# Kernel tuning notes

Hardware: AMD Instinct MI355X
Metric: run time of the kernel (lower is better)

The kernel has to match this reference:

```python
import jax, jax.numpy as jnp
import numpy as np

N_NODES = 10000
N_EDGES = 640000
IN_FEATS = 256
H_FEATS = 128
NUM_CLASSES = 64


def _kaiming(key, shape):
    fan_in = shape[1]
    std = np.sqrt(2.0 / fan_in)
    return jax.random.normal(key, shape, dtype=jnp.float32) * std


def setup_inputs() -> dict:
    key = jax.random.key(0)
    ks = jax.random.split(key, 10)
    x = jax.random.normal(ks[0], (N_NODES, IN_FEATS), dtype=jnp.float32)
    edge_index = jax.random.randint(ks[1], (2, N_EDGES), 0, N_NODES, dtype=jnp.int64)
    return {
        "x": x,
        "edge_index": edge_index,
        "W_lin": _kaiming(ks[2], (H_FEATS, IN_FEATS)),
        "b_lin": jnp.zeros((H_FEATS,), jnp.float32),
        "Wl1": _kaiming(ks[3], (H_FEATS, H_FEATS)),
        "bl1": jnp.zeros((H_FEATS,), jnp.float32),
        "Wr1": _kaiming(ks[4], (H_FEATS, H_FEATS)),
        "Wl2": _kaiming(ks[5], (H_FEATS, H_FEATS)),
        "bl2": jnp.zeros((H_FEATS,), jnp.float32),
        "Wr2": _kaiming(ks[6], (H_FEATS, H_FEATS)),
        "W_cls": _kaiming(ks[7], (NUM_CLASSES, H_FEATS)),
    }


def _sage_conv(x, src, dst, Wl, bl, Wr, n_nodes):
    # PyG SAGEConv (mean aggr): out = lin_l(mean_{j->i} x_j) + lin_r(x_i)
    msg = x[src]                                    # [E, H] gather
    agg = jax.ops.segment_sum(msg, dst, num_segments=n_nodes)  # [N, H]
    deg = jax.ops.segment_sum(jnp.ones((src.shape[0],), x.dtype), dst,
                              num_segments=n_nodes)            # [N]
    mean = agg / jnp.maximum(deg, 1.0)[:, None]
    return mean @ Wl.T + bl + x @ Wr.T


def reference(x, edge_index, W_lin, b_lin, Wl1, bl1, Wr1, Wl2, bl2, Wr2, W_cls):
    src, dst = edge_index[0], edge_index[1]
    n = x.shape[0]
    h = jax.nn.relu(x @ W_lin.T + b_lin)            # input projection + relu
    h = _sage_conv(h, src, dst, Wl1, bl1, Wr1, n)   # sage1 (no relu: linear is truthy)
    h = _sage_conv(h, src, dst, Wl2, bl2, Wr2, n)   # sage2
    h = jax.nn.relu(h)
    return h @ W_cls.T                              # weight.mm(x.t()).t()
```

## Files before the change

kernel.cpp:

```cpp
#include <hip/hip_runtime.h>

#define NN 10000
#define HF 128
#define INF_ 256
#define CLS 64
#define NR 8
#define SEG 32
#define CAPT (NR * SEG)
#define NP 10240
#define RT  (NN / 16)
#define NPB 8
#define NB  (NN / NPB)
#define LDP (HF + 8)

typedef __attribute__((ext_vector_type(8))) short short8;
typedef __attribute__((ext_vector_type(4))) float f32x4;

__device__ __forceinline__ unsigned short f2bf(float f) {
    unsigned u = __builtin_bit_cast(unsigned, f);
    u = (u + 0x7fffu + ((u >> 16) & 1u)) >> 16;
    return (unsigned short)u;
}
__device__ __forceinline__ float bfbits2f(unsigned u) {
    u <<= 16;
    return __builtin_bit_cast(float, u);
}


template <int K, int NC>
__device__ __forceinline__
void mfma_rows16(int row0, int col0,
                 const unsigned short* __restrict__ A, int lda,
                 const unsigned short* __restrict__ W, f32x4* acc) {
    int lane = threadIdx.x & 63;
    int m = lane & 15, quad = lane >> 4;
    const unsigned short* arow = A + (size_t)(row0 + m) * lda + quad * 8;
    const short8* bp[NC];
#pragma unroll
    for (int c = 0; c < NC; ++c)
        bp[c] = (const short8*)(W + (size_t)(col0 + c * 16 + m) * K + quad * 8);
#pragma unroll
    for (int k0 = 0; k0 < K; k0 += 32) {
        short8 a = *(const short8*)(arow + k0);
#pragma unroll
        for (int c = 0; c < NC; ++c)
            acc[c] = __builtin_amdgcn_mfma_f32_16x16x32_bf16(a, bp[c][k0 >> 3], acc[c], 0, 0, 0);
    }
}

__device__ __forceinline__ short8 pack8(float4 a, float4 b) {
    short8 r;
    r[0] = (short)f2bf(a.x); r[1] = (short)f2bf(a.y);
    r[2] = (short)f2bf(a.z); r[3] = (short)f2bf(a.w);
    r[4] = (short)f2bf(b.x); r[5] = (short)f2bf(b.y);
    r[6] = (short)f2bf(b.z); r[7] = (short)f2bf(b.w);
    return r;
}

__device__ __forceinline__
void gemm1_wave(int row_tile, int col0, const float* __restrict__ x,
                const float* __restrict__ Wlin, const float* __restrict__ blin,
                unsigned short* __restrict__ h0) {
    int lane = threadIdx.x & 63;
    int m = lane & 15, quad = lane >> 4;
    const float* ar = x    + (size_t)(row_tile * 16 + m) * INF_ + quad * 8;
    const float* w0 = Wlin + (size_t)(col0 +  0 + m) * INF_ + quad * 8;
    const float* w1 = Wlin + (size_t)(col0 + 16 + m) * INF_ + quad * 8;
    const float* w2 = Wlin + (size_t)(col0 + 32 + m) * INF_ + quad * 8;
    const float* w3 = Wlin + (size_t)(col0 + 48 + m) * INF_ + quad * 8;
    f32x4 acc[4] = {};
#pragma unroll
    for (int k0 = 0; k0 < INF_; k0 += 32) {
        short8 a  = pack8(*(const float4*)(ar + k0), *(const float4*)(ar + k0 + 4));
        short8 b0 = pack8(*(const float4*)(w0 + k0), *(const float4*)(w0 + k0 + 4));
        short8 b1 = pack8(*(const float4*)(w1 + k0), *(const float4*)(w1 + k0 + 4));
        short8 b2 = pack8(*(const float4*)(w2 + k0), *(const float4*)(w2 + k0 + 4));
        short8 b3 = pack8(*(const float4*)(w3 + k0), *(const float4*)(w3 + k0 + 4));
        acc[0] = __builtin_amdgcn_mfma_f32_16x16x32_bf16(a, b0, acc[0], 0, 0, 0);
        acc[1] = __builtin_amdgcn_mfma_f32_16x16x32_bf16(a, b1, acc[1], 0, 0, 0);
        acc[2] = __builtin_amdgcn_mfma_f32_16x16x32_bf16(a, b2, acc[2], 0, 0, 0);
        acc[3] = __builtin_amdgcn_mfma_f32_16x16x32_bf16(a, b3, acc[3], 0, 0, 0);
    }
#pragma unroll
    for (int c = 0; c < 4; ++c) {
        int colg = col0 + c * 16 + m;
        float bv = blin[colg];
#pragma unroll
        for (int r = 0; r < 4; ++r) {
            int rowg = row_tile * 16 + quad * 4 + r;
            h0[(size_t)rowg * HF + colg] = f2bf(fmaxf(acc[c][r] + bv, 0.f));
        }
    }
}

#define GB 313
#define FB 2500
#define CB 288

__global__ __launch_bounds__(256)
void fused_k(const float* __restrict__ x, const float* __restrict__ Wlin,
             const float* __restrict__ blin, unsigned short* __restrict__ h0,
             const int* __restrict__ src, const int* __restrict__ dst,
             int* __restrict__ cnt8, unsigned short* __restrict__ colb, int E,
             const float* __restrict__ Wl1, const float* __restrict__ Wr1,
             const float* __restrict__ Wl2, const float* __restrict__ Wr2,
             const float* __restrict__ Wcls, unsigned short* __restrict__ wb) {
    int b = blockIdx.x;
    if (b < GB) {
        int wave = threadIdx.x >> 6;
        int row_tile = b * 2 + (wave >> 1);
        if (row_tile >= RT) return;
        gemm1_wave(row_tile, (wave & 1) * 64, x, Wlin, blin, h0);
    } else if (b < GB + FB) {
        int r = b & 7;
        int i = (b - GB) * 256 + threadIdx.x;
        if (i < E) {
            int d = dst[i];
            int pos = atomicAdd(&cnt8[r * NP + d], 1);
            if (pos < SEG) colb[(size_t)d * CAPT + r * SEG + pos] = (unsigned short)src[i];
        }
    } else {
        int i = (b - GB - FB) * 256 + threadIdx.x;
        const float* s; int off;
        if      (i < 16384) { s = Wl1;  off = 0; }
        else if (i < 32768) { s = Wr1;  off = 16384; }
        else if (i < 49152) { s = Wl2;  off = 32768; }
        else if (i < 65536) { s = Wr2;  off = 49152; }
        else if (i < 73728) { s = Wcls; off = 65536; }
        else return;
        wb[i] = f2bf(s[i - off]);
    }
}

__device__ __forceinline__
void gather_mean(const unsigned short* __restrict__ h,
                 const int* __restrict__ cnt8, int node,
                 const unsigned short* __restrict__ seg,
                 unsigned short* __restrict__ cols,
                 unsigned short* __restrict__ msrow) {
    int lane = threadIdx.x & 63;
    int q   = lane >> 4;
    int r16 = lane & 15;

    int craw0 = 0;
    if (lane < 8) craw0 = cnt8[lane * NP + node];
    int c0 = craw0 > SEG ? SEG : craw0;
    int off0 = 0, deg = 0, cdeg = 0;
#pragma unroll
    for (int i = 0; i < 8; ++i) {
        int ci = __shfl(c0, i);
        int ri = __shfl(craw0, i);
        if (lane > i) off0 += ci;
        cdeg += ci;
        deg  += ri;
    }
#pragma unroll
    for (int p = 0; p < 4; ++p) {
        int r = 2 * p + (lane >> 5);
        int j = lane & 31;
        unsigned short v = seg[r * SEG + j];
        int cr  = __shfl(c0, r);
        int orr = __shfl(off0, r);
        if (j < cr) cols[orr + j] = v;
    }

    const uint4* __restrict__ hp = (const uint4*)h;
    float a0 = 0.f, a1 = 0.f, a2 = 0.f, a3 = 0.f;
    float a4 = 0.f, a5 = 0.f, a6 = 0.f, a7 = 0.f;
#pragma unroll 4
    for (int e0 = 0; e0 < cdeg; e0 += 4) {
        int e = e0 + q;
        if (e < cdeg) {
            int s = (int)cols[e];
            uint4 v = hp[(size_t)s * 16 + r16];
            a0 += bfbits2f(v.x & 0xffffu); a1 += bfbits2f(v.x >> 16);
            a2 += bfbits2f(v.y & 0xffffu); a3 += bfbits2f(v.y >> 16);
            a4 += bfbits2f(v.z & 0xffffu); a5 += bfbits2f(v.z >> 16);
            a6 += bfbits2f(v.w & 0xffffu); a7 += bfbits2f(v.w >> 16);
        }
    }
    a0 += __shfl_xor(a0, 16); a0 += __shfl_xor(a0, 32);
    a1 += __shfl_xor(a1, 16); a1 += __shfl_xor(a1, 32);
    a2 += __shfl_xor(a2, 16); a2 += __shfl_xor(a2, 32);
    a3 += __shfl_xor(a3, 16); a3 += __shfl_xor(a3, 32);
    a4 += __shfl_xor(a4, 16); a4 += __shfl_xor(a4, 32);
    a5 += __shfl_xor(a5, 16); a5 += __shfl_xor(a5, 32);
    a6 += __shfl_xor(a6, 16); a6 += __shfl_xor(a6, 32);
    a7 += __shfl_xor(a7, 16); a7 += __shfl_xor(a7, 32);
    if (q == 0) {
        float inv = (deg > 0) ? 1.0f / (float)deg : 0.f;
        uint4 o;
        o.x = (unsigned)f2bf(a0 * inv) | ((unsigned)f2bf(a1 * inv) << 16);
        o.y = (unsigned)f2bf(a2 * inv) | ((unsigned)f2bf(a3 * inv) << 16);
        o.z = (unsigned)f2bf(a4 * inv) | ((unsigned)f2bf(a5 * inv) << 16);
        o.w = (unsigned)f2bf(a6 * inv) | ((unsigned)f2bf(a7 * inv) << 16);
        ((uint4*)msrow)[r16] = o;
    }
}

__global__ __launch_bounds__(512)
void aggfin1_k(const unsigned short* __restrict__ h0, const int* __restrict__ cnt8,
               const unsigned short* __restrict__ colb,
               const unsigned short* __restrict__ Wr, const unsigned short* __restrict__ Wl,
               const float* __restrict__ bias, unsigned short* __restrict__ h1) {
    __shared__ __align__(16) unsigned short ms[16][LDP];
    __shared__ __align__(16) unsigned short colsLds[NPB][CAPT];
    int wave = threadIdx.x >> 6;
    int lane = threadIdx.x & 63;
    int m = lane & 15, quad = lane >> 4;
    int row0 = blockIdx.x * NPB;
    int node = row0 + wave;
    gather_mean(h0, cnt8, node, colb + (size_t)node * CAPT,
                &colsLds[wave][0], &ms[wave][0]);

    f32x4 acc[1] = {};
    mfma_rows16<HF, 1>(row0, wave * 16, h0, HF, Wr, acc);
    __syncthreads();
    mfma_rows16<HF, 1>(0, wave * 16, &ms[0][0], LDP, Wl, acc);
    if (quad < 2) {
        int colg = wave * 16 + m;
        float bv = bias[colg];
#pragma unroll
        for (int r = 0; r < 4; ++r) {
            int rowg = row0 + quad * 4 + r;
            h1[(size_t)rowg * HF + colg] = f2bf(acc[0][r] + bv);
        }
    }
}

__global__ __launch_bounds__(512)
void aggfin2cls_k(const unsigned short* __restrict__ h1, const int* __restrict__ cnt8,
                  const unsigned short* __restrict__ colb,
                  const unsigned short* __restrict__ Wr, const unsigned short* __restrict__ Wl,
                  const float* __restrict__ bias, const unsigned short* __restrict__ Wc,
                  float* __restrict__ out) {
    __shared__ __align__(16) unsigned short ms[16][LDP];
    __shared__ __align__(16) unsigned short h2s[16][LDP];
    __shared__ __align__(16) unsigned short colsLds[NPB][CAPT];
    int wave = threadIdx.x >> 6;
    int lane = threadIdx.x & 63;
    int m = lane & 15, quad = lane >> 4;
    int row0 = blockIdx.x * NPB;
    int node = row0 + wave;
    gather_mean(h1, cnt8, node, colb + (size_t)node * CAPT,
                &colsLds[wave][0], &ms[wave][0]);

    f32x4 acc[1] = {};
    mfma_rows16<HF, 1>(row0, wave * 16, h1, HF, Wr, acc);
    __syncthreads();
    mfma_rows16<HF, 1>(0, wave * 16, &ms[0][0], LDP, Wl, acc);
    {
        int colg = wave * 16 + m;
        float bv = bias[colg];
#pragma unroll
        for (int r = 0; r < 4; ++r) {
            h2s[quad * 4 + r][colg] = f2bf(fmaxf(acc[0][r] + bv, 0.f));
        }
    }
    __syncthreads();
    if (wave < 4) {
        f32x4 cacc[1] = {};
        mfma_rows16<HF, 1>(0, wave * 16, &h2s[0][0], LDP, Wc, cacc);
        if (quad < 2) {
            int colg = wave * 16 + m;
#pragma unroll
            for (int r = 0; r < 4; ++r) {
                int rowg = row0 + quad * 4 + r;
                out[(size_t)rowg * CLS + colg] = cacc[0][r];
            }
        }
    }
}


extern "C" void kernel_launch(void* const* d_in, const int* in_sizes, int n_in,
                              void* d_out, int out_size, void* d_ws, size_t ws_size,
                              hipStream_t stream) {
    const float* x      = (const float*)d_in[0];
    const int*   ei     = (const int*)d_in[1];
    const float* W_lin  = (const float*)d_in[2];
    const float* b_lin  = (const float*)d_in[3];
    const float* Wl1    = (const float*)d_in[4];
    const float* bl1    = (const float*)d_in[5];
    const float* Wr1    = (const float*)d_in[6];
    const float* Wl2    = (const float*)d_in[7];
    const float* bl2    = (const float*)d_in[8];
    const float* Wr2    = (const float*)d_in[9];
    const float* W_cls  = (const float*)d_in[10];
    float* out = (float*)d_out;

    const int E = in_sizes[1] / 2;
    const int* src = ei;
    const int* dst = ei + E;

    unsigned short* wb  = (unsigned short*)d_ws;
    unsigned short* wbl1 = wb;
    unsigned short* wbr1 = wb + 16384;
    unsigned short* wbl2 = wb + 32768;
    unsigned short* wbr2 = wb + 49152;
    unsigned short* wbc  = wb + 65536;
    unsigned short* h0  = wb + 73728;
    unsigned short* h1  = h0 + (size_t)(NN + 16) * HF;
    int* cnt8 = (int*)(h1 + (size_t)(NN + 16) * HF);
    unsigned short* colb = (unsigned short*)(cnt8 + NR * NP);

    hipMemsetAsync(cnt8, 0, NR * NP * sizeof(int), stream);

    fused_k<<<GB + FB + CB, 256, 0, stream>>>(
        x, W_lin, b_lin, h0, src, dst, cnt8, colb, E,
        Wl1, Wr1, Wl2, Wr2, W_cls, wb);

    aggfin1_k<<<NB, 512, 0, stream>>>(h0, cnt8, colb, wbr1, wbl1, bl1, h1);

    aggfin2cls_k<<<NB, 512, 0, stream>>>(h1, cnt8, colb, wbr2, wbl2, bl2, wbc, out);
}
```

Baseline: 176.3 us.

## Process 16 nodes per block with two interleaved gathers per wave

Each 512-thread block now handles 16 nodes instead of 8, with each wave gathering and averaging neighbor features for two nodes in an interleaved loop. The 16-row MFMA tiles are now fully used instead of half-wasted, and the block count is halved. The interleaving puts more independent loads in flight per wave, at the cost of more registers and load imbalance between the paired nodes. The h0/h1 padding was removed because 10000 divides evenly by 16.

```diff
diff --git a/kernel.cpp b/kernel.cpp
--- a/kernel.cpp
+++ b/kernel.cpp
@@ -9,8 +9,6 @@
 #define CAPT (NR * SEG)
 #define NP 10240
 #define RT  (NN / 16)
-#define NPB 8
-#define NB  (NN / NPB)
 #define LDP (HF + 8)
 
 typedef __attribute__((ext_vector_type(8))) short short8;
@@ -29,12 +27,12 @@
 
 template <int K, int NC>
 __device__ __forceinline__
-void mfma_rows16(int row0, int col0,
-                 const unsigned short* __restrict__ A, int lda,
-                 const unsigned short* __restrict__ W, f32x4* acc) {
+void mfma_cols(int row_tile, int col0,
+               const unsigned short* __restrict__ A, int lda,
+               const unsigned short* __restrict__ W, f32x4* acc) {
     int lane = threadIdx.x & 63;
     int m = lane & 15, quad = lane >> 4;
-    const unsigned short* arow = A + (size_t)(row0 + m) * lda + quad * 8;
+    const unsigned short* arow = A + (size_t)(row_tile * 16 + m) * lda + quad * 8;
     const short8* bp[NC];
 #pragma unroll
     for (int c = 0; c < NC; ++c)
@@ -133,19 +131,14 @@
 }
 
 __device__ __forceinline__
-void gather_mean(const unsigned short* __restrict__ h,
-                 const int* __restrict__ cnt8, int node,
-                 const unsigned short* __restrict__ seg,
-                 unsigned short* __restrict__ cols,
-                 unsigned short* __restrict__ msrow) {
-    int lane = threadIdx.x & 63;
-    int q   = lane >> 4;
-    int r16 = lane & 15;
-
+void compact_node(const int* __restrict__ cnt8, int node,
+                  const unsigned short* __restrict__ seg,
+                  unsigned short* __restrict__ cols, int& cdeg, int& deg) {
+    int lane = threadIdx.x & 63;
     int craw0 = 0;
     if (lane < 8) craw0 = cnt8[lane * NP + node];
     int c0 = craw0 > SEG ? SEG : craw0;
-    int off0 = 0, deg = 0, cdeg = 0;
+    int off0 = 0; cdeg = 0; deg = 0;
 #pragma unroll
     for (int i = 0; i < 8; ++i) {
         int ci = __shfl(c0, i);
@@ -163,20 +156,45 @@
         int orr = __shfl(off0, r);
         if (j < cr) cols[orr + j] = v;
     }
+}
+
+__device__ __forceinline__
+void gather2(const unsigned short* __restrict__ h,
+             const int* __restrict__ cnt8, int nodeA, int nodeB,
+             const unsigned short* __restrict__ colb,
+             unsigned short* __restrict__ colsA, unsigned short* __restrict__ colsB,
+             unsigned short* __restrict__ msA, unsigned short* __restrict__ msB) {
+    int lane = threadIdx.x & 63;
+    int q   = lane >> 4;
+    int r16 = lane & 15;
+    int cdA, dgA, cdB, dgB;
+    compact_node(cnt8, nodeA, colb + (size_t)nodeA * CAPT, colsA, cdA, dgA);
+    compact_node(cnt8, nodeB, colb + (size_t)nodeB * CAPT, colsB, cdB, dgB);
 
     const uint4* __restrict__ hp = (const uint4*)h;
     float a0 = 0.f, a1 = 0.f, a2 = 0.f, a3 = 0.f;
     float a4 = 0.f, a5 = 0.f, a6 = 0.f, a7 = 0.f;
+    float b0 = 0.f, b1 = 0.f, b2 = 0.f, b3 = 0.f;
+    float b4 = 0.f, b5 = 0.f, b6 = 0.f, b7 = 0.f;
+    int cdmax = cdA > cdB ? cdA : cdB;
 #pragma unroll 4
-    for (int e0 = 0; e0 < cdeg; e0 += 4) {
+    for (int e0 = 0; e0 < cdmax; e0 += 4) {
         int e = e0 + q;
-        if (e < cdeg) {
-            int s = (int)cols[e];
+        if (e < cdA) {
+            int s = (int)colsA[e];
             uint4 v = hp[(size_t)s * 16 + r16];
             a0 += bfbits2f(v.x & 0xffffu); a1 += bfbits2f(v.x >> 16);
             a2 += bfbits2f(v.y & 0xffffu); a3 += bfbits2f(v.y >> 16);
             a4 += bfbits2f(v.z & 0xffffu); a5 += bfbits2f(v.z >> 16);
             a6 += bfbits2f(v.w & 0xffffu); a7 += bfbits2f(v.w >> 16);
+        }
+        if (e < cdB) {
+            int s = (int)colsB[e];
+            uint4 v = hp[(size_t)s * 16 + r16];
+            b0 += bfbits2f(v.x & 0xffffu); b1 += bfbits2f(v.x >> 16);
+            b2 += bfbits2f(v.y & 0xffffu); b3 += bfbits2f(v.y >> 16);
+            b4 += bfbits2f(v.z & 0xffffu); b5 += bfbits2f(v.z >> 16);
+            b6 += bfbits2f(v.w & 0xffffu); b7 += bfbits2f(v.w >> 16);
         }
     }
     a0 += __shfl_xor(a0, 16); a0 += __shfl_xor(a0, 32);
@@ -187,14 +205,28 @@
     a5 += __shfl_xor(a5, 16); a5 += __shfl_xor(a5, 32);
     a6 += __shfl_xor(a6, 16); a6 += __shfl_xor(a6, 32);
     a7 += __shfl_xor(a7, 16); a7 += __shfl_xor(a7, 32);
+    b0 += __shfl_xor(b0, 16); b0 += __shfl_xor(b0, 32);
+    b1 += __shfl_xor(b1, 16); b1 += __shfl_xor(b1, 32);
+    b2 += __shfl_xor(b2, 16); b2 += __shfl_xor(b2, 32);
+    b3 += __shfl_xor(b3, 16); b3 += __shfl_xor(b3, 32);
+    b4 += __shfl_xor(b4, 16); b4 += __shfl_xor(b4, 32);
+    b5 += __shfl_xor(b5, 16); b5 += __shfl_xor(b5, 32);
+    b6 += __shfl_xor(b6, 16); b6 += __shfl_xor(b6, 32);
+    b7 += __shfl_xor(b7, 16); b7 += __shfl_xor(b7, 32);
     if (q == 0) {
-        float inv = (deg > 0) ? 1.0f / (float)deg : 0.f;
-        uint4 o;
-        o.x = (unsigned)f2bf(a0 * inv) | ((unsigned)f2bf(a1 * inv) << 16);
-        o.y = (unsigned)f2bf(a2 * inv) | ((unsigned)f2bf(a3 * inv) << 16);
-        o.z = (unsigned)f2bf(a4 * inv) | ((unsigned)f2bf(a5 * inv) << 16);
-        o.w = (unsigned)f2bf(a6 * inv) | ((unsigned)f2bf(a7 * inv) << 16);
-        ((uint4*)msrow)[r16] = o;
+        float ia = (dgA > 0) ? 1.0f / (float)dgA : 0.f;
+        float ib = (dgB > 0) ? 1.0f / (float)dgB : 0.f;
+        uint4 oa, ob;
+        oa.x = (unsigned)f2bf(a0 * ia) | ((unsigned)f2bf(a1 * ia) << 16);
+        oa.y = (unsigned)f2bf(a2 * ia) | ((unsigned)f2bf(a3 * ia) << 16);
+        oa.z = (unsigned)f2bf(a4 * ia) | ((unsigned)f2bf(a5 * ia) << 16);
+        oa.w = (unsigned)f2bf(a6 * ia) | ((unsigned)f2bf(a7 * ia) << 16);
+        ob.x = (unsigned)f2bf(b0 * ib) | ((unsigned)f2bf(b1 * ib) << 16);
+        ob.y = (unsigned)f2bf(b2 * ib) | ((unsigned)f2bf(b3 * ib) << 16);
+        ob.z = (unsigned)f2bf(b4 * ib) | ((unsigned)f2bf(b5 * ib) << 16);
+        ob.w = (unsigned)f2bf(b6 * ib) | ((unsigned)f2bf(b7 * ib) << 16);
+        ((uint4*)msA)[r16] = oa;
+        ((uint4*)msB)[r16] = ob;
     }
 }
 
@@ -204,25 +236,25 @@
                const unsigned short* __restrict__ Wr, const unsigned short* __restrict__ Wl,
                const float* __restrict__ bias, unsigned short* __restrict__ h1) {
     __shared__ __align__(16) unsigned short ms[16][LDP];
-    __shared__ __align__(16) unsigned short colsLds[NPB][CAPT];
+    __shared__ __align__(16) unsigned short colsLds[16][CAPT];
     int wave = threadIdx.x >> 6;
-    int lane = threadIdx.x & 63;
-    int m = lane & 15, quad = lane >> 4;
-    int row0 = blockIdx.x * NPB;
-    int node = row0 + wave;
-    gather_mean(h0, cnt8, node, colb + (size_t)node * CAPT,
-                &colsLds[wave][0], &ms[wave][0]);
+    int nodeA = blockIdx.x * 16 + wave * 2;
+    gather2(h0, cnt8, nodeA, nodeA + 1, colb,
+            &colsLds[wave * 2][0], &colsLds[wave * 2 + 1][0],
+            &ms[wave * 2][0], &ms[wave * 2 + 1][0]);
 
     f32x4 acc[1] = {};
-    mfma_rows16<HF, 1>(row0, wave * 16, h0, HF, Wr, acc);
+    mfma_cols<HF, 1>(blockIdx.x, wave * 16, h0, HF, Wr, acc);
     __syncthreads();
-    mfma_rows16<HF, 1>(0, wave * 16, &ms[0][0], LDP, Wl, acc);
-    if (quad < 2) {
+    mfma_cols<HF, 1>(0, wave * 16, &ms[0][0], LDP, Wl, acc);
+    {
+        int lane = threadIdx.x & 63;
+        int m = lane & 15, quad = lane >> 4;
         int colg = wave * 16 + m;
         float bv = bias[colg];
 #pragma unroll
         for (int r = 0; r < 4; ++r) {
-            int rowg = row0 + quad * 4 + r;
+            int rowg = blockIdx.x * 16 + quad * 4 + r;
             h1[(size_t)rowg * HF + colg] = f2bf(acc[0][r] + bv);
         }
     }
@@ -236,38 +268,37 @@
                   float* __restrict__ out) {
     __shared__ __align__(16) unsigned short ms[16][LDP];
     __shared__ __align__(16) unsigned short h2s[16][LDP];
-    __shared__ __align__(16) unsigned short colsLds[NPB][CAPT];
+    __shared__ __align__(16) unsigned short colsLds[16][CAPT];
     int wave = threadIdx.x >> 6;
     int lane = threadIdx.x & 63;
     int m = lane & 15, quad = lane >> 4;
-    int row0 = blockIdx.x * NPB;
-    int node = row0 + wave;
-    gather_mean(h1, cnt8, node, colb + (size_t)node * CAPT,
-                &colsLds[wave][0], &ms[wave][0]);
+    int nodeA = blockIdx.x * 16 + wave * 2;
+    gather2(h1, cnt8, nodeA, nodeA + 1, colb,
+            &colsLds[wave * 2][0], &colsLds[wave * 2 + 1][0],
+            &ms[wave * 2][0], &ms[wave * 2 + 1][0]);
 
     f32x4 acc[1] = {};
-    mfma_rows16<HF, 1>(row0, wave * 16, h1, HF, Wr, acc);
+    mfma_cols<HF, 1>(blockIdx.x, wave * 16, h1, HF, Wr, acc);
     __syncthreads();
-    mfma_rows16<HF, 1>(0, wave * 16, &ms[0][0], LDP, Wl, acc);
+    mfma_cols<HF, 1>(0, wave * 16, &ms[0][0], LDP, Wl, acc);
     {
         int colg = wave * 16 + m;
         float bv = bias[colg];
 #pragma unroll
         for (int r = 0; r < 4; ++r) {
-            h2s[quad * 4 + r][colg] = f2bf(fmaxf(acc[0][r] + bv, 0.f));
+            float v = acc[0][r] + bv;
+            h2s[quad * 4 + r][colg] = f2bf(fmaxf(v, 0.f));
         }
     }
     __syncthreads();
     if (wave < 4) {
         f32x4 cacc[1] = {};
-        mfma_rows16<HF, 1>(0, wave * 16, &h2s[0][0], LDP, Wc, cacc);
-        if (quad < 2) {
-            int colg = wave * 16 + m;
-#pragma unroll
-            for (int r = 0; r < 4; ++r) {
-                int rowg = row0 + quad * 4 + r;
-                out[(size_t)rowg * CLS + colg] = cacc[0][r];
-            }
+        mfma_cols<HF, 1>(0, wave * 16, &h2s[0][0], LDP, Wc, cacc);
+        int colg = wave * 16 + m;
+#pragma unroll
+        for (int r = 0; r < 4; ++r) {
+            int rowg = blockIdx.x * 16 + quad * 4 + r;
+            out[(size_t)rowg * CLS + colg] = cacc[0][r];
         }
     }
 }
@@ -300,8 +331,8 @@
     unsigned short* wbr2 = wb + 49152;
     unsigned short* wbc  = wb + 65536;
     unsigned short* h0  = wb + 73728;
-    unsigned short* h1  = h0 + (size_t)(NN + 16) * HF;
-    int* cnt8 = (int*)(h1 + (size_t)(NN + 16) * HF);
+    unsigned short* h1  = h0 + (size_t)NN * HF;
+    int* cnt8 = (int*)(h1 + (size_t)NN * HF);
     unsigned short* colb = (unsigned short*)(cnt8 + NR * NP);
 
     hipMemsetAsync(cnt8, 0, NR * NP * sizeof(int), stream);
@@ -310,7 +341,7 @@
         x, W_lin, b_lin, h0, src, dst, cnt8, colb, E,
         Wl1, Wr1, Wl2, Wr2, W_cls, wb);
 
-    aggfin1_k<<<NB, 512, 0, stream>>>(h0, cnt8, colb, wbr1, wbl1, bl1, h1);
-
-    aggfin2cls_k<<<NB, 512, 0, stream>>>(h1, cnt8, colb, wbr2, wbl2, bl2, wbc, out);
-}
+    aggfin1_k<<<RT, 512, 0, stream>>>(h0, cnt8, colb, wbr1, wbl1, bl1, h1);
+
+    aggfin2cls_k<<<RT, 512, 0, stream>>>(h1, cnt8, colb, wbr2, wbl2, bl2, wbc, out);
+}
```

Result: faster. 164.0 us (-7.0%).
